# Performance work log

Measured on AMD Instinct MI355X. Metric: run time of the kernel, lower is better.

Reference implementation:

```python
import jax, jax.numpy as jnp
import numpy as np
import math

B, L, D, H = 4, 2048, 512, 8
DH = D // H
MAX_SEQ = 2048


def setup_inputs() -> dict:
    key = jax.random.key(0)
    ks = jax.random.split(key, 12)
    s = 1.0 / math.sqrt(D)
    return {
        "q_in": jax.random.normal(ks[0], (B, L, D), jnp.float32),
        "k_in": jax.random.normal(ks[1], (B, L, D), jnp.float32),
        "v_in": jax.random.normal(ks[2], (B, L, D), jnp.float32),
        "Wq_w": jax.random.normal(ks[3], (D, D), jnp.float32) * s,
        "Wq_b": jnp.zeros((D,), jnp.float32),
        "Wk_w": jax.random.normal(ks[4], (D, D), jnp.float32) * s,
        "Wk_b": jnp.zeros((D,), jnp.float32),
        "Wv_w": jax.random.normal(ks[5], (D, D), jnp.float32) * s,
        "Wv_b": jnp.zeros((D,), jnp.float32),
        "E": jax.random.normal(ks[6], (MAX_SEQ, DH), jnp.float32) * (1.0 / math.sqrt(DH)),
        "fc_w": jax.random.normal(ks[7], (D, D), jnp.float32) * s,
        "fc_b": jnp.zeros((D,), jnp.float32),
    }


def _forward(q_in, k_in, v_in, Wq_w, Wq_b, Wk_w, Wk_b, Wv_w, Wv_b, E, fc_w, fc_b):
    b, lq, d = q_in.shape
    dh = E.shape[1]
    h = d // dh

    def proj(x, W, bias):
        # [b, l, d] -> [b, h, l, dh]
        y = x @ W + bias
        return y.reshape(b, -1, h, dh).transpose(0, 2, 1, 3)

    q = proj(q_in, Wq_w, Wq_b)
    k = proj(k_in, Wk_w, Wk_b)
    v = proj(v_in, Wv_w, Wv_b)
    len_q, len_k = q.shape[2], k.shape[2]

    # left-aligned relative embedding slice
    max_seq = E.shape[0]
    start = max(0, max_seq - len_q)
    e = E[start:, :]                       # [m, dh], m = min(max_seq, len_q)
    m = e.shape[0]

    QE = jnp.einsum("bhld,md->bhlm", q, e)  # [b, h, l, m]
    # qe masking: for query row i keep columns j with i + j >= m - 1
    keep = (jnp.arange(len_q)[:, None] + jnp.arange(m)[None, :]) >= (m - 1)
    QE = QE * keep.astype(QE.dtype)

    # skewing trick: pad one zero column on the left, reshape, drop first row
    padded = jnp.pad(QE, ((0, 0), (0, 0), (0, 0), (1, 0)))  # [b, h, l, m+1]
    reshaped = padded.reshape(b, h, m + 1, len_q)
    Srel = reshaped[:, :, 1:, :]           # [b, h, m, l]
    if len_k > len_q:
        Srel = jnp.pad(Srel, ((0, 0), (0, 0), (0, 0), (0, len_k - len_q)))
    elif len_k < len_q:
        Srel = Srel[:, :, :, :len_k]

    QKt = jnp.einsum("bhld,bhsd->bhls", q, k)
    logits = (QKt + Srel) / math.sqrt(dh)
    attn_w = jax.nn.softmax(logits, axis=-1)
    attn = jnp.einsum("bhls,bhsd->bhld", attn_w, v)
    out = attn.transpose(0, 2, 1, 3).reshape(b, -1, d)
    out = out @ fc_w + fc_b
    return out, attn_w


def reference(q_in, k_in, v_in, Wq_w, Wq_b, Wk_w, Wk_b, Wv_w, Wv_b, E, fc_w, fc_b):
    return _forward(q_in, k_in, v_in, Wq_w, Wq_b, Wk_w, Wk_b, Wv_w, Wv_b, E, fc_w, fc_b)
```

## Files before the change

### kernel.cpp

```cpp
#include <hip/hip_runtime.h>

#define SC2   0.18033688011112042f
#define PSTR  36

typedef __attribute__((ext_vector_type(8)))  __bf16       bf16x8;
typedef __attribute__((ext_vector_type(16))) float        f32x16;
typedef __attribute__((ext_vector_type(4)))  float        f32x4;
typedef __attribute__((ext_vector_type(4)))  unsigned int u32x4;
typedef __attribute__((ext_vector_type(2)))  unsigned int u32x2;

#define ROWPAT(g, hi) ((((g)&3)) + 8*((g)>>2) + 4*(hi))

__device__ inline unsigned short f2bf(float f){
  unsigned u = __builtin_bit_cast(unsigned, f);
  u += 0x7FFFu + ((u >> 16) & 1u);
  return (unsigned short)(u >> 16);
}
__device__ inline float bf2f(unsigned short h){
  unsigned u = ((unsigned)h) << 16;
  return __builtin_bit_cast(float, u);
}
__device__ inline unsigned pack2bf(float lo, float hi){
  return (unsigned)f2bf(lo) | ((unsigned)f2bf(hi) << 16);
}
__device__ inline f32x16 zero16(){
  f32x16 z;
  #pragma unroll
  for (int i=0;i<16;i++) z[i]=0.f;
  return z;
}

__global__ __launch_bounds__(256) void transpose_w_kernel(const float* __restrict__ W,
                                                          unsigned short* __restrict__ Wt){
  __shared__ unsigned short t[32][33];
  const int n0 = blockIdx.x*32, k0 = blockIdx.y*32;
  const int tx = threadIdx.x & 31, ty = threadIdx.x >> 5;
  #pragma unroll
  for (int i=0;i<4;i++){
    int k = ty*4 + i;
    t[k][tx] = f2bf(W[(size_t)(k0+k)*512 + n0+tx]);
  }
  __syncthreads();
  #pragma unroll
  for (int i=0;i<4;i++){
    int n = ty*4+i;
    Wt[(size_t)(n0+n)*512 + k0 + tx] = t[tx][n];
  }
}

__global__ __launch_bounds__(256) void transpose_v_kernel(const unsigned short* __restrict__ V,
                                                          unsigned short* __restrict__ VT){
  __shared__ unsigned short t[32][33];
  const int bh = blockIdx.z;
  const int l0 = blockIdx.x*32, d0 = blockIdx.y*32;
  const int tx = threadIdx.x & 31, ty = threadIdx.x >> 5;
  const unsigned short* Vb = V + (size_t)bh*2048*64;
  unsigned short* Tb = VT + (size_t)bh*64*2048;
  #pragma unroll
  for (int i=0;i<4;i++){
    int row = ty*4+i;
    t[row][tx] = Vb[(size_t)(l0+row)*64 + d0+tx];
  }
  __syncthreads();
  #pragma unroll
  for (int i=0;i<4;i++){
    int d = ty*4+i;
    Tb[(size_t)(d0+d)*2048 + l0+tx] = t[tx][d];
  }
}

__global__ __launch_bounds__(256) void erev_kernel(const float* __restrict__ E,
                                                   unsigned short* __restrict__ Ebf){
  const int i = blockIdx.x*256 + threadIdx.x;
  const int base = i*4;
  const int u = base >> 6, d = base & 63;
  f32x4 v = *(const f32x4*)(E + (size_t)(2047 - u)*64 + d);
  unsigned short o[4];
  #pragma unroll
  for (int j=0;j<4;j++) o[j] = f2bf(v[j]);
  *(u32x2*)(Ebf + (size_t)u*64 + d) = u32x2{(unsigned)o[0] | ((unsigned)o[1]<<16),
                                            (unsigned)o[2] | ((unsigned)o[3]<<16)};
}

__global__ __launch_bounds__(256,2) void proj_gemm_kernel(
    const float* __restrict__ X, const unsigned int* __restrict__ Wt,
    const float* __restrict__ bias, unsigned short* __restrict__ Y)
{
  __shared__ unsigned int Al[128][17];
  __shared__ unsigned int Bl[128][17];
  const int n0 = blockIdx.x * 128;
  const int m0 = blockIdx.y * 128;
  const int tid = threadIdx.x;
  const int lane = tid & 63, wave = tid >> 6;
  const int lr = lane & 31, hi = lane >> 5;
  const int wr = wave >> 1, wc = wave & 1;
  const int r = tid & 127, kh = tid >> 7;

  f32x16 acc[2][2];
  acc[0][0]=zero16(); acc[0][1]=zero16(); acc[1][0]=zero16(); acc[1][1]=zero16();

  for (int k0=0; k0<512; k0+=32){
    const float* Xr = X + (size_t)(m0 + r)*512 + k0 + kh*16;
    #pragma unroll
    for (int c=0;c<2;c++){
      f32x4 x0 = *(const f32x4*)(Xr + c*8);
      f32x4 x1 = *(const f32x4*)(Xr + c*8 + 4);
      Al[r][kh*8 + c*4 + 0] = pack2bf(x0[0], x0[1]);
      Al[r][kh*8 + c*4 + 1] = pack2bf(x0[2], x0[3]);
      Al[r][kh*8 + c*4 + 2] = pack2bf(x1[0], x1[1]);
      Al[r][kh*8 + c*4 + 3] = pack2bf(x1[2], x1[3]);
    }
    const unsigned int* Wr = Wt + (size_t)(n0 + r)*256 + (k0>>1) + kh*8;
    #pragma unroll
    for (int c=0;c<8;c++) Bl[r][kh*8 + c] = Wr[c];
    __syncthreads();
    #pragma unroll
    for (int t=0;t<2;t++){
      bf16x8 af[2], bfr[2];
      #pragma unroll
      for (int mt=0;mt<2;mt++){
        u32x4 w;
        #pragma unroll
        for (int j=0;j<4;j++) w[j] = Al[wr*64 + mt*32 + lr][t*8 + hi*4 + j];
        af[mt] = __builtin_bit_cast(bf16x8, w);
      }
      #pragma unroll
      for (int nt=0;nt<2;nt++){
        u32x4 w;
        #pragma unroll
        for (int j=0;j<4;j++) w[j] = Bl[wc*64 + nt*32 + lr][t*8 + hi*4 + j];
        bfr[nt] = __builtin_bit_cast(bf16x8, w);
      }
      #pragma unroll
      for (int mt=0;mt<2;mt++)
        #pragma unroll
        for (int nt=0;nt<2;nt++)
          acc[mt][nt] = __builtin_amdgcn_mfma_f32_32x32x16_bf16(af[mt], bfr[nt], acc[mt][nt], 0,0,0);
    }
    __syncthreads();
  }

  #pragma unroll
  for (int mt=0;mt<2;mt++)
    #pragma unroll
    for (int nt=0;nt<2;nt++){
      const int n = n0 + wc*64 + nt*32 + lr;
      const float bv = bias[n];
      const int h = n >> 6, dh = n & 63;
      #pragma unroll
      for (int g=0; g<16; g++){
        const int m = m0 + wr*64 + mt*32 + ROWPAT(g,hi);
        const int b = m >> 11, l = m & 2047;
        Y[((size_t)(b*8 + h)*2048 + l)*64 + dh] = f2bf(acc[mt][nt][g] + bv);
      }
    }
}

__global__ __launch_bounds__(64) void attn_kernel(
    const unsigned short* __restrict__ Q,
    const unsigned short* __restrict__ Kb,
    const unsigned short* __restrict__ VT,
    const unsigned short* __restrict__ Ebf,
    float* __restrict__ attn_w,
    unsigned short* __restrict__ attn_o)
{
  __shared__ unsigned short slab[3*32*PSTR];
  const int tid = threadIdx.x;
  const int lane = tid & 63;
  const int lr = lane & 31;
  const int hi = lane >> 5;

  const int bid = blockIdx.x;
  const int xcd = bid & 7;
  const int j   = bid >> 3;
  const int bhg = xcd*4 + (j >> 6);
  const int ltile = 63 - (j & 63);
  const int l0w = ltile*32;
  const int c_max = ltile;

  unsigned short* Wa = slab;
  unsigned short* Wb = Wa + 32*PSTR;
  unsigned short* Ps = Wb + 32*PSTR;

  const unsigned short* Qrow = Q + ((size_t)bhg*2048 + l0w + lr)*64;
  bf16x8 qf[4];
  #pragma unroll
  for (int t=0;t<4;t++) qf[t] = *(const bf16x8*)(Qrow + t*16 + hi*8);

  const unsigned short* Krows = Kb + (size_t)bhg*2048*64;
  const unsigned short* Vtb   = VT + (size_t)bhg*64*2048;

  float dpart[16];
  #pragma unroll
  for (int g=0;g<16;g++) dpart[g] = 0.f;

  #pragma unroll 2
  for (int c = c_max+1; c < 64; ++c){
    const int s0 = c*32;
    f32x16 acc = zero16();
    const unsigned short* Krow = Krows + (size_t)(s0 + lr)*64;
    #pragma unroll
    for (int t=0;t<4;t++){
      bf16x8 kf = *(const bf16x8*)(Krow + t*16 + hi*8);
      acc = __builtin_amdgcn_mfma_f32_32x32x16_bf16(qf[t], kf, acc, 0,0,0);
    }
    #pragma unroll
    for (int g=0; g<16; g++) dpart[g] += exp2f(acc[g] * SC2);
  }
  {
    unsigned short* cur = Wa;
    unsigned short* prv = Wb;
    #pragma unroll 1
    for (int c = c_max; c >= 0; --c){
      const int s0 = c*32;
      const int delta = l0w - s0;
      {
        const unsigned short* Erow = Ebf + (size_t)(delta + lr)*64;
        f32x16 eacc = zero16();
        #pragma unroll
        for (int t=0;t<4;t++){
          bf16x8 ef = *(const bf16x8*)(Erow + t*16 + hi*8);
          eacc = __builtin_amdgcn_mfma_f32_32x32x16_bf16(qf[t], ef, eacc, 0,0,0);
        }
        #pragma unroll
        for (int g=0; g<16; g++) cur[ROWPAT(g,hi)*PSTR + lr] = f2bf(eacc[g]);
      }
      f32x16 acc = zero16();
      const unsigned short* Krow = Krows + (size_t)(s0 + lr)*64;
      #pragma unroll
      for (int t=0;t<4;t++){
        bf16x8 kf = *(const bf16x8*)(Krow + t*16 + hi*8);
        acc = __builtin_amdgcn_mfma_f32_32x32x16_bf16(qf[t], kf, acc, 0,0,0);
      }
      #pragma unroll
      for (int g=0; g<16; g++){
        const int rp = ROWPAT(g,hi);
        const int dloc = rp - lr;
        float v = acc[g];
        if (delta + dloc >= 0)
          v += bf2f(dloc >= 0 ? cur[rp*PSTR + dloc] : prv[rp*PSTR + 32 + dloc]);
        dpart[g] += exp2f(v * SC2);
      }
      unsigned short* tmp = cur; cur = prv; prv = tmp;
    }
  }
  float invd[16];
  #pragma unroll
  for (int g=0; g<16; g++){
    float v = dpart[g];
    v += __shfl_xor(v, 1, 64);
    v += __shfl_xor(v, 2, 64);
    v += __shfl_xor(v, 4, 64);
    v += __shfl_xor(v, 8, 64);
    v += __shfl_xor(v, 16, 64);
    invd[g] = 1.0f / v;
  }

  f32x16 oacc[2];
  oacc[0]=zero16(); oacc[1]=zero16();
  float* awbase = attn_w + ((size_t)bhg*2048 + l0w)*2048;

  #pragma unroll 1
  for (int half=0; half<2; ++half){
    unsigned short* cur = Wa;
    unsigned short* prv = Wb;
    const int cbeg = half ? c_max+1 : c_max;
    const int cend = half ? 64 : -1;
    const int cstp = half ? 1 : -1;
    #pragma unroll 1
    for (int c = cbeg; c != cend; c += cstp){
      const int s0 = c*32;
      const int delta = l0w - s0;
      if (!half){
        const unsigned short* Erow = Ebf + (size_t)(delta + lr)*64;
        f32x16 eacc = zero16();
        #pragma unroll
        for (int t=0;t<4;t++){
          bf16x8 ef = *(const bf16x8*)(Erow + t*16 + hi*8);
          eacc = __builtin_amdgcn_mfma_f32_32x32x16_bf16(qf[t], ef, eacc, 0,0,0);
        }
        #pragma unroll
        for (int g=0; g<16; g++) cur[ROWPAT(g,hi)*PSTR + lr] = f2bf(eacc[g]);
      }
      f32x16 acc = zero16();
      const unsigned short* Krow = Krows + (size_t)(s0 + lr)*64;
      #pragma unroll
      for (int t=0;t<4;t++){
        bf16x8 kf = *(const bf16x8*)(Krow + t*16 + hi*8);
        acc = __builtin_amdgcn_mfma_f32_32x32x16_bf16(qf[t], kf, acc, 0,0,0);
      }
      float p[16];
      #pragma unroll
      for (int g=0; g<16; g++){
        const int rp = ROWPAT(g,hi);
        float v = acc[g];
        if (!half){
          const int dloc = rp - lr;
          if (delta + dloc >= 0)
            v += bf2f(dloc >= 0 ? cur[rp*PSTR + dloc] : prv[rp*PSTR + 32 + dloc]);
        }
        p[g] = exp2f(v * SC2) * invd[g];
        __builtin_nontemporal_store(p[g], awbase + (size_t)rp*2048 + s0 + lr);
      }
      #pragma unroll
      for (int q=0;q<8;q++){
        const int rp0 = ROWPAT(2*q,hi);
        const unsigned pkv = pack2bf(p[2*q], p[2*q+1]);
        Ps[rp0*PSTR + lr]     = (unsigned short)(pkv & 0xFFFFu);
        Ps[(rp0+1)*PSTR + lr] = (unsigned short)(pkv >> 16);
      }
      bf16x8 af[2];
      #pragma unroll
      for (int sh=0; sh<2; sh++){
        const unsigned short* ap = Ps + lr*PSTR + sh*16 + 8*hi;
        u32x2 a0 = *(const u32x2*)(ap);
        u32x2 a1 = *(const u32x2*)(ap + 4);
        u32x4 w; w[0]=a0[0]; w[1]=a0[1]; w[2]=a1[0]; w[3]=a1[1];
        af[sh] = __builtin_bit_cast(bf16x8, w);
      }
      #pragma unroll
      for (int sh=0; sh<2; sh++)
        #pragma unroll
        for (int dt=0; dt<2; dt++){
          bf16x8 vfr = *(const bf16x8*)(Vtb + (size_t)(dt*32+lr)*2048 + s0 + sh*16 + 8*hi);
          oacc[dt] = __builtin_amdgcn_mfma_f32_32x32x16_bf16(af[sh], vfr, oacc[dt], 0,0,0);
        }
      if (!half){ unsigned short* tmp = cur; cur = prv; prv = tmp; }
    }
  }

  unsigned short* Obase = attn_o + ((size_t)bhg*2048 + l0w)*64;
  #pragma unroll
  for (int dt=0; dt<2; dt++)
    #pragma unroll
    for (int g=0; g<16; g++){
      const int rp = ROWPAT(g,hi);
      Obase[(size_t)rp*64 + dt*32 + lr] = f2bf(oacc[dt][g]);
    }
}

__global__ __launch_bounds__(256,2) void fc_gemm_kernel(
    const unsigned short* __restrict__ A,
    const unsigned int* __restrict__ Wt,
    const float* __restrict__ bias, float* __restrict__ Out)
{
  __shared__ unsigned int Al[128][17];
  __shared__ unsigned int Bl[128][17];
  const int n0 = blockIdx.x * 128;
  const int m0 = blockIdx.y * 128;
  const int tid = threadIdx.x;
  const int lane = tid & 63, wave = tid >> 6;
  const int lr = lane & 31, hi = lane >> 5;
  const int wr = wave >> 1, wc = wave & 1;
  const int r = tid & 127, kh = tid >> 7;

  f32x16 acc[2][2];
  acc[0][0]=zero16(); acc[0][1]=zero16(); acc[1][0]=zero16(); acc[1][1]=zero16();

  for (int k0=0; k0<512; k0+=32){
    const int m = m0 + r; const int b = m >> 11, l = m & 2047;
    const int k = k0 + kh*16; const int h = k >> 6, dh0 = k & 63;
    const unsigned int* Ar = (const unsigned int*)(A + ((size_t)(b*8+h)*2048 + l)*64 + dh0);
    #pragma unroll
    for (int c=0;c<8;c++) Al[r][kh*8+c] = Ar[c];
    const unsigned int* Wr = Wt + (size_t)(n0 + r)*256 + (k0>>1) + kh*8;
    #pragma unroll
    for (int c=0;c<8;c++) Bl[r][kh*8 + c] = Wr[c];
    __syncthreads();
    #pragma unroll
    for (int t=0;t<2;t++){
      bf16x8 af[2], bfr[2];
      #pragma unroll
      for (int mt=0;mt<2;mt++){
        u32x4 w;
        #pragma unroll
        for (int j=0;j<4;j++) w[j] = Al[wr*64 + mt*32 + lr][t*8 + hi*4 + j];
        af[mt] = __builtin_bit_cast(bf16x8, w);
      }
      #pragma unroll
      for (int nt=0;nt<2;nt++){
        u32x4 w;
        #pragma unroll
        for (int j=0;j<4;j++) w[j] = Bl[wc*64 + nt*32 + lr][t*8 + hi*4 + j];
        bfr[nt] = __builtin_bit_cast(bf16x8, w);
      }
      #pragma unroll
      for (int mt=0;mt<2;mt++)
        #pragma unroll
        for (int nt=0;nt<2;nt++)
          acc[mt][nt] = __builtin_amdgcn_mfma_f32_32x32x16_bf16(af[mt], bfr[nt], acc[mt][nt], 0,0,0);
    }
    __syncthreads();
  }

  #pragma unroll
  for (int mt=0;mt<2;mt++)
    #pragma unroll
    for (int nt=0;nt<2;nt++){
      const int n = n0 + wc*64 + nt*32 + lr;
      const float bv = bias[n];
      #pragma unroll
      for (int g=0; g<16; g++){
        const int m2 = m0 + wr*64 + mt*32 + ROWPAT(g,hi);
        Out[(size_t)m2*512 + n] = acc[mt][nt][g] + bv;
      }
    }
}

extern "C" void kernel_launch(void* const* d_in, const int* in_sizes, int n_in,
                              void* d_out, int out_size, void* d_ws, size_t ws_size,
                              hipStream_t stream)
{
  const float* q_in = (const float*)d_in[0];
  const float* k_in = (const float*)d_in[1];
  const float* v_in = (const float*)d_in[2];
  const float* Wq_w = (const float*)d_in[3];
  const float* Wq_b = (const float*)d_in[4];
  const float* Wk_w = (const float*)d_in[5];
  const float* Wk_b = (const float*)d_in[6];
  const float* Wv_w = (const float*)d_in[7];
  const float* Wv_b = (const float*)d_in[8];
  const float* E    = (const float*)d_in[9];
  const float* fc_w = (const float*)d_in[10];
  const float* fc_b = (const float*)d_in[11];

  float* out = (float*)d_out;
  float* attn_w = out + (size_t)4*2048*512;

  unsigned short* Qws = (unsigned short*)d_ws;
  unsigned short* Kws = Qws + (size_t)4194304;
  unsigned short* Vws = Kws + (size_t)4194304;
  unsigned short* ATT = Vws + (size_t)4194304;
  unsigned short* VTs = ATT + (size_t)4194304;
  unsigned short* Ebf = VTs + (size_t)4194304;
  unsigned short* WqT = Ebf + 131072;
  unsigned short* WkT = WqT + 262144;
  unsigned short* WvT = WkT + 262144;
  unsigned short* WfT = WvT + 262144;

  dim3 tg(16,16);
  hipLaunchKernelGGL(transpose_w_kernel, tg, dim3(256), 0, stream, Wq_w, WqT);
  hipLaunchKernelGGL(transpose_w_kernel, tg, dim3(256), 0, stream, Wk_w, WkT);
  hipLaunchKernelGGL(transpose_w_kernel, tg, dim3(256), 0, stream, Wv_w, WvT);
  hipLaunchKernelGGL(transpose_w_kernel, tg, dim3(256), 0, stream, fc_w, WfT);
  hipLaunchKernelGGL(erev_kernel, dim3(128), dim3(256), 0, stream, E, Ebf);

  dim3 pg(4, 64);
  hipLaunchKernelGGL(proj_gemm_kernel, pg, dim3(256), 0, stream, q_in, (const unsigned int*)WqT, Wq_b, Qws);
  hipLaunchKernelGGL(proj_gemm_kernel, pg, dim3(256), 0, stream, k_in, (const unsigned int*)WkT, Wk_b, Kws);
  hipLaunchKernelGGL(proj_gemm_kernel, pg, dim3(256), 0, stream, v_in, (const unsigned int*)WvT, Wv_b, Vws);

  hipLaunchKernelGGL(transpose_v_kernel, dim3(64,2,32), dim3(256), 0, stream, Vws, VTs);

  hipLaunchKernelGGL(attn_kernel, dim3(2048), dim3(64), 0, stream, Qws, Kws, VTs, Ebf, attn_w, ATT);

  hipLaunchKernelGGL(fc_gemm_kernel, pg, dim3(256), 0, stream, ATT, (const unsigned int*)WfT, fc_b, out);
}
```

Baseline: 460.3 us.

## Split attention key range across four waves with register-cached probabilities

The attention kernel now runs four waves per block, each covering a quarter of the key tiles. Each wave keeps its bf16-packed probabilities in registers so QK^T and the relative-embedding terms are computed once rather than twice. Row sums are combined through shared memory, and per-wave partial PV outputs go to an fp32 workspace that a new merge kernel sums into bf16. The three projection GEMMs are merged into one launch, and V^T gets a tiled layout. The cost is a large register array (pk[16][8]), extra global traffic for the partial outputs, one extra kernel launch, and attn_w values rounded through bf16 before normalisation.

```diff
diff --git a/kernel.cpp b/kernel.cpp
--- a/kernel.cpp
+++ b/kernel.cpp
@@ -65,7 +65,7 @@
   #pragma unroll
   for (int i=0;i<4;i++){
     int d = ty*4+i;
-    Tb[(size_t)(d0+d)*2048 + l0+tx] = t[tx][d];
+    Tb[(size_t)(l0>>5)*2048 + (size_t)(d0+d)*32 + tx] = t[tx][d];
   }
 }
 
@@ -82,10 +82,18 @@
                                             (unsigned)o[2] | ((unsigned)o[3]<<16)};
 }
 
-__global__ __launch_bounds__(256,2) void proj_gemm_kernel(
-    const float* __restrict__ X, const unsigned int* __restrict__ Wt,
-    const float* __restrict__ bias, unsigned short* __restrict__ Y)
+__global__ __launch_bounds__(256,2) void proj3_gemm_kernel(
+    const float* __restrict__ X0, const float* __restrict__ X1, const float* __restrict__ X2,
+    const unsigned int* __restrict__ W0, const unsigned int* __restrict__ W1, const unsigned int* __restrict__ W2,
+    const float* __restrict__ b0, const float* __restrict__ b1, const float* __restrict__ b2,
+    unsigned short* __restrict__ Y0, unsigned short* __restrict__ Y1, unsigned short* __restrict__ Y2)
 {
+  const int z = blockIdx.z;
+  const float* X = z==0 ? X0 : (z==1 ? X1 : X2);
+  const unsigned int* Wt = z==0 ? W0 : (z==1 ? W1 : W2);
+  const float* bias = z==0 ? b0 : (z==1 ? b1 : b2);
+  unsigned short* Y = z==0 ? Y0 : (z==1 ? Y1 : Y2);
+
   __shared__ unsigned int Al[128][17];
   __shared__ unsigned int Bl[128][17];
   const int n0 = blockIdx.x * 128;
@@ -156,16 +164,20 @@
     }
 }
 
-__global__ __launch_bounds__(64) void attn_kernel(
+__global__ void attn_fused_kernel(
     const unsigned short* __restrict__ Q,
     const unsigned short* __restrict__ Kb,
     const unsigned short* __restrict__ VT,
     const unsigned short* __restrict__ Ebf,
     float* __restrict__ attn_w,
-    unsigned short* __restrict__ attn_o)
+    float* __restrict__ po)
 {
-  __shared__ unsigned short slab[3*32*PSTR];
+  __shared__ unsigned short Wab[4][2][32*PSTR];
+  __shared__ unsigned short Psb[4][32*PSTR];
+  __shared__ float Sd[4][32];
+
   const int tid = threadIdx.x;
+  const int wave = tid >> 6;
   const int lane = tid & 63;
   const int lr = lane & 31;
   const int hi = lane >> 5;
@@ -174,13 +186,17 @@
   const int xcd = bid & 7;
   const int j   = bid >> 3;
   const int bhg = xcd*4 + (j >> 6);
-  const int ltile = 63 - (j & 63);
+  const int jj  = j & 63;
+  const int ltile = 63 - jj;
   const int l0w = ltile*32;
   const int c_max = ltile;
-
-  unsigned short* Wa = slab;
-  unsigned short* Wb = Wa + 32*PSTR;
-  unsigned short* Ps = Wb + 32*PSTR;
+  const int quarter = wave;
+  const int clo = quarter*16, chi = clo + 15;
+  const int relhi = c_max < chi ? c_max : chi;
+
+  unsigned short* cur = Wab[wave][0];
+  unsigned short* prv = Wab[wave][1];
+  unsigned short* Ps  = Psb[wave];
 
   const unsigned short* Qrow = Q + ((size_t)bhg*2048 + l0w + lr)*64;
   bf16x8 qf[4];
@@ -193,29 +209,28 @@
   float dpart[16];
   #pragma unroll
   for (int g=0;g<16;g++) dpart[g] = 0.f;
-
-  #pragma unroll 2
-  for (int c = c_max+1; c < 64; ++c){
-    const int s0 = c*32;
+  unsigned pk[16][8];
+
+  #pragma unroll
+  for (int cc = 15; cc >= 0; --cc){
+    const int c = clo + cc;
     f32x16 acc = zero16();
-    const unsigned short* Krow = Krows + (size_t)(s0 + lr)*64;
-    #pragma unroll
-    for (int t=0;t<4;t++){
-      bf16x8 kf = *(const bf16x8*)(Krow + t*16 + hi*8);
-      acc = __builtin_amdgcn_mfma_f32_32x32x16_bf16(qf[t], kf, acc, 0,0,0);
-    }
-    #pragma unroll
-    for (int g=0; g<16; g++) dpart[g] += exp2f(acc[g] * SC2);
-  }
-  {
-    unsigned short* cur = Wa;
-    unsigned short* prv = Wb;
-    #pragma unroll 1
-    for (int c = c_max; c >= 0; --c){
-      const int s0 = c*32;
-      const int delta = l0w - s0;
-      {
-        const unsigned short* Erow = Ebf + (size_t)(delta + lr)*64;
+    {
+      const unsigned short* Krow = Krows + (size_t)(c*32 + lr)*64;
+      #pragma unroll
+      for (int t=0;t<4;t++){
+        bf16x8 kf = *(const bf16x8*)(Krow + t*16 + hi*8);
+        acc = __builtin_amdgcn_mfma_f32_32x32x16_bf16(qf[t], kf, acc, 0,0,0);
+      }
+    }
+    float p[16];
+    if (c > c_max){
+      #pragma unroll
+      for (int g=0; g<16; g++) p[g] = exp2f(acc[g] * SC2);
+    } else {
+      if (c == relhi && relhi < c_max){
+        const int dpr = l0w - 32*(relhi+1);
+        const unsigned short* Erow = Ebf + (size_t)(dpr + lr)*64;
         f32x16 eacc = zero16();
         #pragma unroll
         for (int t=0;t<4;t++){
@@ -223,14 +238,19 @@
           eacc = __builtin_amdgcn_mfma_f32_32x32x16_bf16(qf[t], ef, eacc, 0,0,0);
         }
         #pragma unroll
+        for (int g=0; g<16; g++) prv[ROWPAT(g,hi)*PSTR + lr] = f2bf(eacc[g]);
+      }
+      const int delta = l0w - c*32;
+      {
+        const unsigned short* Erow = Ebf + (size_t)(delta + lr)*64;
+        f32x16 eacc = zero16();
+        #pragma unroll
+        for (int t=0;t<4;t++){
+          bf16x8 ef = *(const bf16x8*)(Erow + t*16 + hi*8);
+          eacc = __builtin_amdgcn_mfma_f32_32x32x16_bf16(qf[t], ef, eacc, 0,0,0);
+        }
+        #pragma unroll
         for (int g=0; g<16; g++) cur[ROWPAT(g,hi)*PSTR + lr] = f2bf(eacc[g]);
-      }
-      f32x16 acc = zero16();
-      const unsigned short* Krow = Krows + (size_t)(s0 + lr)*64;
-      #pragma unroll
-      for (int t=0;t<4;t++){
-        bf16x8 kf = *(const bf16x8*)(Krow + t*16 + hi*8);
-        acc = __builtin_amdgcn_mfma_f32_32x32x16_bf16(qf[t], kf, acc, 0,0,0);
       }
       #pragma unroll
       for (int g=0; g<16; g++){
@@ -239,12 +259,16 @@
         float v = acc[g];
         if (delta + dloc >= 0)
           v += bf2f(dloc >= 0 ? cur[rp*PSTR + dloc] : prv[rp*PSTR + 32 + dloc]);
-        dpart[g] += exp2f(v * SC2);
+        p[g] = exp2f(v * SC2);
       }
       unsigned short* tmp = cur; cur = prv; prv = tmp;
     }
-  }
-  float invd[16];
+    #pragma unroll
+    for (int g=0; g<16; g++) dpart[g] += p[g];
+    #pragma unroll
+    for (int q2=0; q2<8; q2++) pk[cc][q2] = pack2bf(p[2*q2], p[2*q2+1]);
+  }
+
   #pragma unroll
   for (int g=0; g<16; g++){
     float v = dpart[g];
@@ -253,90 +277,84 @@
     v += __shfl_xor(v, 4, 64);
     v += __shfl_xor(v, 8, 64);
     v += __shfl_xor(v, 16, 64);
-    invd[g] = 1.0f / v;
+    dpart[g] = v;
+  }
+  if (lr == 0){
+    #pragma unroll
+    for (int g=0; g<16; g++) Sd[wave][ROWPAT(g,hi)] = dpart[g];
+  }
+  __syncthreads();
+  float invd[16];
+  #pragma unroll
+  for (int g=0; g<16; g++){
+    const int rp = ROWPAT(g,hi);
+    invd[g] = 1.0f / (Sd[0][rp] + Sd[1][rp] + Sd[2][rp] + Sd[3][rp]);
   }
 
   f32x16 oacc[2];
   oacc[0]=zero16(); oacc[1]=zero16();
   float* awbase = attn_w + ((size_t)bhg*2048 + l0w)*2048;
 
-  #pragma unroll 1
-  for (int half=0; half<2; ++half){
-    unsigned short* cur = Wa;
-    unsigned short* prv = Wb;
-    const int cbeg = half ? c_max+1 : c_max;
-    const int cend = half ? 64 : -1;
-    const int cstp = half ? 1 : -1;
-    #pragma unroll 1
-    for (int c = cbeg; c != cend; c += cstp){
-      const int s0 = c*32;
-      const int delta = l0w - s0;
-      if (!half){
-        const unsigned short* Erow = Ebf + (size_t)(delta + lr)*64;
-        f32x16 eacc = zero16();
-        #pragma unroll
-        for (int t=0;t<4;t++){
-          bf16x8 ef = *(const bf16x8*)(Erow + t*16 + hi*8);
-          eacc = __builtin_amdgcn_mfma_f32_32x32x16_bf16(qf[t], ef, eacc, 0,0,0);
-        }
-        #pragma unroll
-        for (int g=0; g<16; g++) cur[ROWPAT(g,hi)*PSTR + lr] = f2bf(eacc[g]);
-      }
-      f32x16 acc = zero16();
-      const unsigned short* Krow = Krows + (size_t)(s0 + lr)*64;
-      #pragma unroll
-      for (int t=0;t<4;t++){
-        bf16x8 kf = *(const bf16x8*)(Krow + t*16 + hi*8);
-        acc = __builtin_amdgcn_mfma_f32_32x32x16_bf16(qf[t], kf, acc, 0,0,0);
-      }
-      float p[16];
-      #pragma unroll
-      for (int g=0; g<16; g++){
-        const int rp = ROWPAT(g,hi);
-        float v = acc[g];
-        if (!half){
-          const int dloc = rp - lr;
-          if (delta + dloc >= 0)
-            v += bf2f(dloc >= 0 ? cur[rp*PSTR + dloc] : prv[rp*PSTR + 32 + dloc]);
-        }
-        p[g] = exp2f(v * SC2) * invd[g];
-        __builtin_nontemporal_store(p[g], awbase + (size_t)rp*2048 + s0 + lr);
-      }
-      #pragma unroll
-      for (int q=0;q<8;q++){
-        const int rp0 = ROWPAT(2*q,hi);
-        const unsigned pkv = pack2bf(p[2*q], p[2*q+1]);
-        Ps[rp0*PSTR + lr]     = (unsigned short)(pkv & 0xFFFFu);
-        Ps[(rp0+1)*PSTR + lr] = (unsigned short)(pkv >> 16);
-      }
-      bf16x8 af[2];
-      #pragma unroll
-      for (int sh=0; sh<2; sh++){
-        const unsigned short* ap = Ps + lr*PSTR + sh*16 + 8*hi;
-        u32x2 a0 = *(const u32x2*)(ap);
-        u32x2 a1 = *(const u32x2*)(ap + 4);
-        u32x4 w; w[0]=a0[0]; w[1]=a0[1]; w[2]=a1[0]; w[3]=a1[1];
-        af[sh] = __builtin_bit_cast(bf16x8, w);
-      }
-      #pragma unroll
-      for (int sh=0; sh<2; sh++)
-        #pragma unroll
-        for (int dt=0; dt<2; dt++){
-          bf16x8 vfr = *(const bf16x8*)(Vtb + (size_t)(dt*32+lr)*2048 + s0 + sh*16 + 8*hi);
-          oacc[dt] = __builtin_amdgcn_mfma_f32_32x32x16_bf16(af[sh], vfr, oacc[dt], 0,0,0);
-        }
-      if (!half){ unsigned short* tmp = cur; cur = prv; prv = tmp; }
-    }
-  }
-
-  unsigned short* Obase = attn_o + ((size_t)bhg*2048 + l0w)*64;
-  #pragma unroll
-  for (int dt=0; dt<2; dt++)
+  #pragma unroll
+  for (int cc = 0; cc < 16; ++cc){
+    const int c = clo + cc;
+    const int s0 = c*32;
     #pragma unroll
     for (int g=0; g<16; g++){
       const int rp = ROWPAT(g,hi);
-      Obase[(size_t)rp*64 + dt*32 + lr] = f2bf(oacc[dt][g]);
-    }
+      const float v = bf2f((unsigned short)((pk[cc][g>>1] >> ((g&1)*16)) & 0xFFFFu)) * invd[g];
+      __builtin_nontemporal_store(v, awbase + (size_t)rp*2048 + s0 + lr);
+    }
+    #pragma unroll
+    for (int q2=0; q2<8; q2++){
+      const int rp0 = ROWPAT(2*q2,hi);
+      Ps[rp0*PSTR + lr]     = (unsigned short)(pk[cc][q2] & 0xFFFFu);
+      Ps[(rp0+1)*PSTR + lr] = (unsigned short)(pk[cc][q2] >> 16);
+    }
+    bf16x8 af[2];
+    #pragma unroll
+    for (int sh=0; sh<2; sh++){
+      const unsigned short* ap = Ps + lr*PSTR + sh*16 + 8*hi;
+      u32x2 a0 = *(const u32x2*)(ap);
+      u32x2 a1 = *(const u32x2*)(ap + 4);
+      u32x4 w; w[0]=a0[0]; w[1]=a0[1]; w[2]=a1[0]; w[3]=a1[1];
+      af[sh] = __builtin_bit_cast(bf16x8, w);
+    }
+    #pragma unroll
+    for (int sh=0; sh<2; sh++)
+      #pragma unroll
+      for (int dt=0; dt<2; dt++){
+        bf16x8 vfr = *(const bf16x8*)(Vtb + (size_t)c*2048 + (size_t)(dt*32+lr)*32 + sh*16 + 8*hi);
+        oacc[dt] = __builtin_amdgcn_mfma_f32_32x32x16_bf16(af[sh], vfr, oacc[dt], 0,0,0);
+      }
+  }
+
+  float* pobase = po + (size_t)quarter*4194304 + ((size_t)bhg*2048 + l0w)*64;
+  #pragma unroll
+  for (int dt=0; dt<2; dt++)
+    #pragma unroll
+    for (int g=0; g<16; g++){
+      const int rp = ROWPAT(g,hi);
+      pobase[(size_t)rp*64 + dt*32 + lr] = oacc[dt][g] * invd[g];
+    }
+}
+
+__global__ __launch_bounds__(256) void pv_merge_kernel(const float* __restrict__ po,
+                                                       unsigned short* __restrict__ ATT){
+  const size_t i = ((size_t)blockIdx.x*256 + threadIdx.x)*8;
+  f32x4 s0 = *(const f32x4*)(po + i);
+  f32x4 s1 = *(const f32x4*)(po + i + 4);
+  #pragma unroll
+  for (int q=1; q<4; q++){
+    s0 += *(const f32x4*)(po + (size_t)q*4194304 + i);
+    s1 += *(const f32x4*)(po + (size_t)q*4194304 + i + 4);
+  }
+  u32x4 w;
+  w[0] = pack2bf(s0[0], s0[1]);
+  w[1] = pack2bf(s0[2], s0[3]);
+  w[2] = pack2bf(s1[0], s1[1]);
+  w[3] = pack2bf(s1[2], s1[3]);
+  *(u32x4*)(ATT + i) = w;
 }
 
 __global__ __launch_bounds__(256,2) void fc_gemm_kernel(
@@ -437,6 +455,7 @@
   unsigned short* WkT = WqT + 262144;
   unsigned short* WvT = WkT + 262144;
   unsigned short* WfT = WvT + 262144;
+  float* po  = (float*)(WfT + 262144);
 
   dim3 tg(16,16);
   hipLaunchKernelGGL(transpose_w_kernel, tg, dim3(256), 0, stream, Wq_w, WqT);
@@ -445,14 +464,17 @@
   hipLaunchKernelGGL(transpose_w_kernel, tg, dim3(256), 0, stream, fc_w, WfT);
   hipLaunchKernelGGL(erev_kernel, dim3(128), dim3(256), 0, stream, E, Ebf);
 
-  dim3 pg(4, 64);
-  hipLaunchKernelGGL(proj_gemm_kernel, pg, dim3(256), 0, stream, q_in, (const unsigned int*)WqT, Wq_b, Qws);
-  hipLaunchKernelGGL(proj_gemm_kernel, pg, dim3(256), 0, stream, k_in, (const unsigned int*)WkT, Wk_b, Kws);
-  hipLaunchKernelGGL(proj_gemm_kernel, pg, dim3(256), 0, stream, v_in, (const unsigned int*)WvT, Wv_b, Vws);
+  hipLaunchKernelGGL(proj3_gemm_kernel, dim3(4,64,3), dim3(256), 0, stream,
+                     q_in, k_in, v_in,
+                     (const unsigned int*)WqT, (const unsigned int*)WkT, (const unsigned int*)WvT,
+                     Wq_b, Wk_b, Wv_b, Qws, Kws, Vws);
 
   hipLaunchKernelGGL(transpose_v_kernel, dim3(64,2,32), dim3(256), 0, stream, Vws, VTs);
 
-  hipLaunchKernelGGL(attn_kernel, dim3(2048), dim3(64), 0, stream, Qws, Kws, VTs, Ebf, attn_w, ATT);
-
-  hipLaunchKernelGGL(fc_gemm_kernel, pg, dim3(256), 0, stream, ATT, (const unsigned int*)WfT, fc_b, out);
-}
+  hipLaunchKernelGGL(attn_fused_kernel, dim3(2048), dim3(256), 0, stream,
+                     Qws, Kws, VTs, Ebf, attn_w, po);
+  hipLaunchKernelGGL(pv_merge_kernel, dim3(2048), dim3(256), 0, stream, po, ATT);
+
+  hipLaunchKernelGGL(fc_gemm_kernel, dim3(4,64), dim3(256), 0, stream,
+                     ATT, (const unsigned int*)WfT, fc_b, out);
+}
```

Result: slower. 1.480 ms (+221.5%).
